# Optimization experiments

Measured on AMD Instinct MI355X. Metric: run time of the kernel, lower is better.

Reference implementation:

```python
import jax, jax.numpy as jnp
import numpy as np

B, D_IN, D_OUT = 8192, 1024, 1024


def setup_inputs() -> dict:
    key = jax.random.key(0)
    k1, k2 = jax.random.split(key)
    x = jax.random.normal(k1, (B, D_IN), dtype=jnp.float32)
    # Keras add_weight(shape=(3, input_dim, output_dim), initializer='uniform')
    kernel = jax.random.normal(k2, (3, D_IN, D_OUT), dtype=jnp.float32) * 0.05
    return {"x": x, "kernel": kernel}


def reference(x, kernel):
    # x: (B, D). Layer does expand_dims(axis=1) -> (B, 1, D) (seq_len == 1).
    output_dim = kernel.shape[-1]
    xe = x[:, None, :]                                   # (B, 1, D)
    q = jnp.einsum('bsd,do->bso', xe, kernel[0])         # (B, 1, O)
    k = jnp.einsum('bsd,do->bso', xe, kernel[1])         # (B, 1, O)
    v = jnp.einsum('bsd,do->bso', xe, kernel[2])         # (B, 1, O)
    scores = jnp.einsum('bqo,bko->bqk', q, k) / jnp.sqrt(
        jnp.asarray(output_dim, x.dtype))                # (B, 1, 1)
    attn = jax.nn.softmax(scores, axis=-1)
    out = jnp.einsum('bqk,bko->bqo', attn, v)            # (B, 1, O)
    return out
```

## Files before the change

### kernel.cpp

```cpp
#include <hip/hip_runtime.h>
#include <hip/hip_bf16.h>
#include <stdint.h>

#define AS1 __attribute__((address_space(1)))
#define AS3 __attribute__((address_space(3)))

typedef __attribute__((ext_vector_type(8))) short bf16x8_t;
typedef __attribute__((ext_vector_type(4))) float f32x4_t;

#define DDIM 1024
#define WT_ELEMS ((size_t)DDIM * DDIM)
#define XB_ELEMS ((size_t)8192 * DDIM)

static __device__ inline ushort f32_to_bf16_rne(float f) {
  union { float f; uint32_t u; } v;
  v.f = f;
  v.u += 0x7FFFu + ((v.u >> 16) & 1u);
  return (ushort)(v.u >> 16);
}

__global__ __launch_bounds__(256) void transpose_w(const float* __restrict__ W,
                                                   ushort* __restrict__ Wt) {
  __shared__ float tile[64][65];
  const int t  = threadIdx.x;
  const int bk = blockIdx.x;
  const int bn = blockIdx.y;
#pragma unroll
  for (int s = 0; s < 4; ++s) {
    const int slot = (s << 8) + t;
    const int r    = slot >> 4;
    const int c4   = (slot & 15) << 2;
    const float4 v = *(const float4*)(W + (size_t)(bk * 64 + r) * DDIM + bn * 64 + c4);
    tile[r][c4 + 0] = v.x; tile[r][c4 + 1] = v.y;
    tile[r][c4 + 2] = v.z; tile[r][c4 + 3] = v.w;
  }
  __syncthreads();
#pragma unroll
  for (int s = 0; s < 2; ++s) {
    const int slot = (s << 8) + t;
    const int n    = slot >> 3;
    const int k8   = (slot & 7) << 3;
    union { ushort h[8]; uint4 u; } tmp;
#pragma unroll
    for (int j = 0; j < 8; ++j) tmp.h[j] = f32_to_bf16_rne(tile[k8 + j][n]);
    *(uint4*)(Wt + (size_t)(bn * 64 + n) * DDIM + bk * 64 + k8) = tmp.u;
  }
}

__global__ __launch_bounds__(256) void convert_x(const float* __restrict__ X,
                                                 ushort* __restrict__ Xb) {
  const size_t i = ((size_t)blockIdx.x * 256 + threadIdx.x) << 3;
  const float4 v0 = *(const float4*)(X + i);
  const float4 v1 = *(const float4*)(X + i + 4);
  union { ushort h[8]; uint4 u; } o;
  o.h[0] = f32_to_bf16_rne(v0.x); o.h[1] = f32_to_bf16_rne(v0.y);
  o.h[2] = f32_to_bf16_rne(v0.z); o.h[3] = f32_to_bf16_rne(v0.w);
  o.h[4] = f32_to_bf16_rne(v1.x); o.h[5] = f32_to_bf16_rne(v1.y);
  o.h[6] = f32_to_bf16_rne(v1.z); o.h[7] = f32_to_bf16_rne(v1.w);
  *(uint4*)(Xb + i) = o.u;
}

__global__ __launch_bounds__(256, 4) void gemm_bb(const ushort* __restrict__ Xb,
                                                  const ushort* __restrict__ Wt,
                                                  float* __restrict__ C) {
  __shared__ __align__(16) ushort As[64 * 32];
  __shared__ __align__(16) ushort Bs[128 * 32];

  const int t    = threadIdx.x;
  const int wave = t >> 6;
  const int lane = t & 63;
  const int m0 = blockIdx.x * 64;
  const int n0 = blockIdx.y * 128;

  const int s  = (wave << 6) + lane;
  const int sr = s >> 2;
  const int sc = (s & 3) ^ ((sr >> 1) & 3);
  const ushort* aptr  = Xb + (size_t)(m0 + sr) * DDIM + (sc << 3);
  const ushort* bptr0 = Wt + (size_t)(n0 + sr) * DDIM + (sc << 3);
  const ushort* bptr1 = Wt + (size_t)(n0 + 64 + sr) * DDIM + (sc << 3);

  AS3 char* ldsA = (AS3 char*)As;
  AS3 char* ldsB = (AS3 char*)Bs;
  const int woff = wave << 10;

  const int wr = (wave >> 1) << 5;
  const int wc = (wave & 1) << 6;
  const int fr = lane & 15;
  const int fq = lane >> 4;

  f32x4_t acc[2][4] = {};

  for (int kt = 0; kt < DDIM; kt += 32) {
    __syncthreads();
    __builtin_amdgcn_global_load_lds((const AS1 void*)aptr,  (AS3 void*)(ldsA + woff),        16, 0, 0);
    __builtin_amdgcn_global_load_lds((const AS1 void*)bptr0, (AS3 void*)(ldsB + woff),        16, 0, 0);
    __builtin_amdgcn_global_load_lds((const AS1 void*)bptr1, (AS3 void*)(ldsB + 4096 + woff), 16, 0, 0);
    aptr += 32; bptr0 += 32; bptr1 += 32;
    __syncthreads();

    bf16x8_t af[2], bfr[4];
#pragma unroll
    for (int mi = 0; mi < 2; ++mi) {
      const int r = wr + (mi << 4) + fr;
      af[mi] = *(const bf16x8_t*)&As[(r << 5) + ((fq ^ ((r >> 1) & 3)) << 3)];
    }
#pragma unroll
    for (int ni = 0; ni < 4; ++ni) {
      const int r = wc + (ni << 4) + fr;
      bfr[ni] = *(const bf16x8_t*)&Bs[(r << 5) + ((fq ^ ((r >> 1) & 3)) << 3)];
    }
#pragma unroll
    for (int mi = 0; mi < 2; ++mi)
#pragma unroll
      for (int ni = 0; ni < 4; ++ni)
        acc[mi][ni] = __builtin_amdgcn_mfma_f32_16x16x32_bf16(af[mi], bfr[ni], acc[mi][ni], 0, 0, 0);
  }

#pragma unroll
  for (int mi = 0; mi < 2; ++mi) {
#pragma unroll
    for (int r = 0; r < 4; ++r) {
      const int row = m0 + wr + (mi << 4) + (fq << 2) + r;
      float* crow = C + (size_t)row * DDIM + n0 + wc + fr;
#pragma unroll
      for (int ni = 0; ni < 4; ++ni)
        crow[ni << 4] = acc[mi][ni][r];
    }
  }
}

__global__ __launch_bounds__(256) void gemm_xw(const float* __restrict__ X,
                                               const ushort* __restrict__ Wt,
                                               float* __restrict__ C) {
  __shared__ __align__(16) ushort As[128 * 32];
  __shared__ __align__(16) ushort Bs[128 * 32];
  const int t    = threadIdx.x;
  const int wave = t >> 6;
  const int lane = t & 63;
  const int m0 = blockIdx.x * 128;
  const int n0 = blockIdx.y * 128;
  const int srow  = (wave << 4) + (lane >> 2);
  const int skcol = (lane & 3) << 3;
  const ushort* bptr0 = Wt + (size_t)(n0 + srow) * DDIM + skcol;
  const ushort* bptr1 = Wt + (size_t)(n0 + 64 + srow) * DDIM + skcol;
  const int ar = t >> 2;
  const int ak = (t & 3) << 3;
  const float* aptr0 = X + (size_t)(m0 + ar) * DDIM + ak;
  const float* aptr1 = X + (size_t)(m0 + 64 + ar) * DDIM + ak;
  ushort* asw0 = &As[(ar << 5) + ak];
  ushort* asw1 = &As[((ar + 64) << 5) + ak];
  const int wr = (wave >> 1) << 6;
  const int wc = (wave & 1) << 6;
  const int fr = lane & 15;
  const int fq = lane >> 4;
  f32x4_t acc[4][4] = {};
  AS3 char* ldsB = (AS3 char*)Bs;
  const int woff = wave << 10;
  for (int kt = 0; kt < DDIM; kt += 32) {
    const float4 a00 = *(const float4*)(aptr0);
    const float4 a01 = *(const float4*)(aptr0 + 4);
    const float4 a10 = *(const float4*)(aptr1);
    const float4 a11 = *(const float4*)(aptr1 + 4);
    aptr0 += 32; aptr1 += 32;
    __syncthreads();
    __builtin_amdgcn_global_load_lds((const AS1 void*)bptr0, (AS3 void*)(ldsB + woff),        16, 0, 0);
    __builtin_amdgcn_global_load_lds((const AS1 void*)bptr1, (AS3 void*)(ldsB + 4096 + woff), 16, 0, 0);
    bptr0 += 32; bptr1 += 32;
    union { ushort h[8]; bf16x8_t v; } c0, c1;
    c0.h[0] = f32_to_bf16_rne(a00.x); c0.h[1] = f32_to_bf16_rne(a00.y);
    c0.h[2] = f32_to_bf16_rne(a00.z); c0.h[3] = f32_to_bf16_rne(a00.w);
    c0.h[4] = f32_to_bf16_rne(a01.x); c0.h[5] = f32_to_bf16_rne(a01.y);
    c0.h[6] = f32_to_bf16_rne(a01.z); c0.h[7] = f32_to_bf16_rne(a01.w);
    c1.h[0] = f32_to_bf16_rne(a10.x); c1.h[1] = f32_to_bf16_rne(a10.y);
    c1.h[2] = f32_to_bf16_rne(a10.z); c1.h[3] = f32_to_bf16_rne(a10.w);
    c1.h[4] = f32_to_bf16_rne(a11.x); c1.h[5] = f32_to_bf16_rne(a11.y);
    c1.h[6] = f32_to_bf16_rne(a11.z); c1.h[7] = f32_to_bf16_rne(a11.w);
    *(bf16x8_t*)asw0 = c0.v;
    *(bf16x8_t*)asw1 = c1.v;
    __syncthreads();
    bf16x8_t af[4], bfr[4];
#pragma unroll
    for (int mi = 0; mi < 4; ++mi)
      af[mi] = *(const bf16x8_t*)&As[((wr + (mi << 4) + fr) << 5) + (fq << 3)];
#pragma unroll
    for (int ni = 0; ni < 4; ++ni)
      bfr[ni] = *(const bf16x8_t*)&Bs[((wc + (ni << 4) + fr) << 5) + (fq << 3)];
#pragma unroll
    for (int mi = 0; mi < 4; ++mi)
#pragma unroll
      for (int ni = 0; ni < 4; ++ni)
        acc[mi][ni] = __builtin_amdgcn_mfma_f32_16x16x32_bf16(af[mi], bfr[ni], acc[mi][ni], 0, 0, 0);
  }
#pragma unroll
  for (int mi = 0; mi < 4; ++mi)
#pragma unroll
    for (int r = 0; r < 4; ++r) {
      const int row = m0 + wr + (mi << 4) + (fq << 2) + r;
      float* crow = C + (size_t)row * DDIM + n0 + wc + fr;
#pragma unroll
      for (int ni = 0; ni < 4; ++ni)
        crow[ni << 4] = acc[mi][ni][r];
    }
}

extern "C" void kernel_launch(void* const* d_in, const int* in_sizes, int n_in,
                              void* d_out, int out_size, void* d_ws, size_t ws_size,
                              hipStream_t stream) {
  const float* x    = (const float*)d_in[0];
  const float* kern = (const float*)d_in[1];
  const float* W = kern + (size_t)2 * DDIM * DDIM;
  ushort* Wt = (ushort*)d_ws;
  const int M = in_sizes[0] / DDIM;

  transpose_w<<<dim3(DDIM / 64, DDIM / 64), 256, 0, stream>>>(W, Wt);

  if (ws_size >= (WT_ELEMS + XB_ELEMS) * sizeof(ushort)) {
    ushort* Xb = (ushort*)d_ws + WT_ELEMS;
    convert_x<<<(unsigned)((size_t)M * DDIM / 8 / 256), 256, 0, stream>>>(x, Xb);
    gemm_bb<<<dim3(M / 64, DDIM / 128), 256, 0, stream>>>(Xb, Wt, (float*)d_out);
  } else {
    gemm_xw<<<dim3(M / 128, DDIM / 128), 256, 0, stream>>>(x, Wt, (float*)d_out);
  }
}
```

Measured before the change: 117.8 us.

## Enlarge bf16 GEMM tile to 128x128 with double-buffered K=64 LDS stages

Moves the bf16 GEMM from 64x128 tiles with K=32 steps to 128x128 tiles with K=64 steps. Global-to-LDS loads for the next stage are issued while the current stage is computed, leaving one barrier per iteration instead of two. The LDS swizzle becomes 8-way to match the wider rows. The aim is more data reuse per loaded byte and less barrier overhead, at the cost of 64KB of LDS per block and lower occupancy.

```diff
diff --git a/kernel.cpp b/kernel.cpp
--- a/kernel.cpp
+++ b/kernel.cpp
@@ -60,64 +60,82 @@
   *(uint4*)(Xb + i) = o.u;
 }
 
-__global__ __launch_bounds__(256, 4) void gemm_bb(const ushort* __restrict__ Xb,
+__global__ __launch_bounds__(256, 2) void gemm_bb(const ushort* __restrict__ Xb,
                                                   const ushort* __restrict__ Wt,
                                                   float* __restrict__ C) {
-  __shared__ __align__(16) ushort As[64 * 32];
-  __shared__ __align__(16) ushort Bs[128 * 32];
+  __shared__ __align__(16) ushort As[2][128 * 64];
+  __shared__ __align__(16) ushort Bs[2][128 * 64];
 
   const int t    = threadIdx.x;
   const int wave = t >> 6;
   const int lane = t & 63;
-  const int m0 = blockIdx.x * 64;
+  const int m0 = blockIdx.x * 128;
   const int n0 = blockIdx.y * 128;
 
-  const int s  = (wave << 6) + lane;
-  const int sr = s >> 2;
-  const int sc = (s & 3) ^ ((sr >> 1) & 3);
-  const ushort* aptr  = Xb + (size_t)(m0 + sr) * DDIM + (sc << 3);
-  const ushort* bptr0 = Wt + (size_t)(n0 + sr) * DDIM + (sc << 3);
-  const ushort* bptr1 = Wt + (size_t)(n0 + 64 + sr) * DDIM + (sc << 3);
-
-  AS3 char* ldsA = (AS3 char*)As;
-  AS3 char* ldsB = (AS3 char*)Bs;
+  const int sr = t >> 3;
+  const int sc = (t & 7) ^ (sr & 7);
+  const ushort* aB = Xb + (size_t)(m0 + sr) * DDIM + (sc << 3);
+  const ushort* bB = Wt + (size_t)(n0 + sr) * DDIM + (sc << 3);
+
+  AS3 char* lA = (AS3 char*)&As[0][0];
+  AS3 char* lB = (AS3 char*)&Bs[0][0];
   const int woff = wave << 10;
 
-  const int wr = (wave >> 1) << 5;
+  const int wr = (wave >> 1) << 6;
   const int wc = (wave & 1) << 6;
   const int fr = lane & 15;
   const int fq = lane >> 4;
 
-  f32x4_t acc[2][4] = {};
-
-  for (int kt = 0; kt < DDIM; kt += 32) {
+  f32x4_t acc[4][4] = {};
+
+  auto issue = [&](int kt, int p) {
+    const ushort* a = aB + kt;
+    const ushort* b = bB + kt;
+    AS3 char* dA = lA + (p << 14) + woff;
+    AS3 char* dB = lB + (p << 14) + woff;
+#pragma unroll
+    for (int j = 0; j < 4; ++j) {
+      __builtin_amdgcn_global_load_lds((const AS1 void*)(a + (size_t)(j << 5) * DDIM),
+                                       (AS3 void*)(dA + (j << 12)), 16, 0, 0);
+      __builtin_amdgcn_global_load_lds((const AS1 void*)(b + (size_t)(j << 5) * DDIM),
+                                       (AS3 void*)(dB + (j << 12)), 16, 0, 0);
+    }
+  };
+
+  issue(0, 0);
+  __syncthreads();
+
+  for (int i = 0; i < 16; ++i) {
+    const int p = i & 1;
+    if (i < 15) issue((i + 1) << 6, p ^ 1);
+
+    const ushort* Ab = &As[p][0];
+    const ushort* Bb = &Bs[p][0];
+#pragma unroll
+    for (int ks = 0; ks < 2; ++ks) {
+      const int kc = (ks << 2) + fq;
+      bf16x8_t af[4], bfr[4];
+#pragma unroll
+      for (int mi = 0; mi < 4; ++mi) {
+        const int r = wr + (mi << 4) + fr;
+        af[mi] = *(const bf16x8_t*)&Ab[(r << 6) + ((kc ^ (r & 7)) << 3)];
+      }
+#pragma unroll
+      for (int ni = 0; ni < 4; ++ni) {
+        const int r = wc + (ni << 4) + fr;
+        bfr[ni] = *(const bf16x8_t*)&Bb[(r << 6) + ((kc ^ (r & 7)) << 3)];
+      }
+#pragma unroll
+      for (int mi = 0; mi < 4; ++mi)
+#pragma unroll
+        for (int ni = 0; ni < 4; ++ni)
+          acc[mi][ni] = __builtin_amdgcn_mfma_f32_16x16x32_bf16(af[mi], bfr[ni], acc[mi][ni], 0, 0, 0);
+    }
     __syncthreads();
-    __builtin_amdgcn_global_load_lds((const AS1 void*)aptr,  (AS3 void*)(ldsA + woff),        16, 0, 0);
-    __builtin_amdgcn_global_load_lds((const AS1 void*)bptr0, (AS3 void*)(ldsB + woff),        16, 0, 0);
-    __builtin_amdgcn_global_load_lds((const AS1 void*)bptr1, (AS3 void*)(ldsB + 4096 + woff), 16, 0, 0);
-    aptr += 32; bptr0 += 32; bptr1 += 32;
-    __syncthreads();
-
-    bf16x8_t af[2], bfr[4];
-#pragma unroll
-    for (int mi = 0; mi < 2; ++mi) {
-      const int r = wr + (mi << 4) + fr;
-      af[mi] = *(const bf16x8_t*)&As[(r << 5) + ((fq ^ ((r >> 1) & 3)) << 3)];
-    }
-#pragma unroll
-    for (int ni = 0; ni < 4; ++ni) {
-      const int r = wc + (ni << 4) + fr;
-      bfr[ni] = *(const bf16x8_t*)&Bs[(r << 5) + ((fq ^ ((r >> 1) & 3)) << 3)];
-    }
-#pragma unroll
-    for (int mi = 0; mi < 2; ++mi)
-#pragma unroll
-      for (int ni = 0; ni < 4; ++ni)
-        acc[mi][ni] = __builtin_amdgcn_mfma_f32_16x16x32_bf16(af[mi], bfr[ni], acc[mi][ni], 0, 0, 0);
-  }
-
-#pragma unroll
-  for (int mi = 0; mi < 2; ++mi) {
+  }
+
+#pragma unroll
+  for (int mi = 0; mi < 4; ++mi) {
 #pragma unroll
     for (int r = 0; r < 4; ++r) {
       const int row = m0 + wr + (mi << 4) + (fq << 2) + r;
@@ -217,7 +235,7 @@
   if (ws_size >= (WT_ELEMS + XB_ELEMS) * sizeof(ushort)) {
     ushort* Xb = (ushort*)d_ws + WT_ELEMS;
     convert_x<<<(unsigned)((size_t)M * DDIM / 8 / 256), 256, 0, stream>>>(x, Xb);
-    gemm_bb<<<dim3(M / 64, DDIM / 128), 256, 0, stream>>>(Xb, Wt, (float*)d_out);
+    gemm_bb<<<dim3(M / 128, DDIM / 128), 256, 0, stream>>>(Xb, Wt, (float*)d_out);
   } else {
     gemm_xw<<<dim3(M / 128, DDIM / 128), 256, 0, stream>>>(x, Wt, (float*)d_out);
   }
```

Result: faster. 111.5 us (-5.4%).

## Pre-swizzle X and W into MFMA fragment layout and load directly to registers

Applied to the files above, without the earlier changes.

Merges the X conversion and the W transpose into one prep kernel. That kernel writes both operands in the per-lane MFMA fragment order. The GEMM then skips LDS and syncthreads: each wave loads its fragments straight from global memory into registers, double-buffered across k-steps, with a 128x128 tile and 4x4 accumulators per wave. The aim is to remove LDS traffic, barriers and one launch. The trade-off is that each wave re-reads fragments from global/L2 with no block-level sharing, and register pressure goes up.

```diff
diff --git a/kernel.cpp b/kernel.cpp
--- a/kernel.cpp
+++ b/kernel.cpp
@@ -17,6 +17,136 @@
   v.f = f;
   v.u += 0x7FFFu + ((v.u >> 16) & 1u);
   return (ushort)(v.u >> 16);
+}
+
+
+__global__ __launch_bounds__(256) void prep(const float* __restrict__ X,
+                                            const float* __restrict__ W,
+                                            ushort* __restrict__ FA,
+                                            ushort* __restrict__ FB,
+                                            int nx) {
+  __shared__ ushort xbuf[16][1032];
+  __shared__ float  wtile[64][65];
+  const int t = threadIdx.x;
+
+  if ((int)blockIdx.x < nx) {
+    const int m16 = blockIdx.x;
+    const float* src = X + (size_t)m16 * 16 * DDIM;
+#pragma unroll
+    for (int rep = 0; rep < 16; ++rep) {
+      const int fl = ((rep << 8) + t) << 2;
+      const float4 v = *(const float4*)(src + fl);
+      const int r = fl >> 10, c = fl & 1023;
+      xbuf[r][c + 0] = f32_to_bf16_rne(v.x);
+      xbuf[r][c + 1] = f32_to_bf16_rne(v.y);
+      xbuf[r][c + 2] = f32_to_bf16_rne(v.z);
+      xbuf[r][c + 3] = f32_to_bf16_rne(v.w);
+    }
+    __syncthreads();
+    ushort* dst = FA + (size_t)m16 * 16384;
+#pragma unroll
+    for (int rep = 0; rep < 8; ++rep) {
+      const int e    = (rep << 8) + t;
+      const int k32  = e >> 6;
+      const int lane = e & 63;
+      const int fr   = lane & 15, fq = lane >> 4;
+      const uint4 u = *(const uint4*)&xbuf[fr][(k32 << 5) + (fq << 3)];
+      *(uint4*)(dst + (size_t)e * 8) = u;
+    }
+    return;
+  }
+
+  const int bid = (int)blockIdx.x - nx;
+  const int bk = bid & 15;
+  const int bn = bid >> 4;
+#pragma unroll
+  for (int s = 0; s < 4; ++s) {
+    const int slot = (s << 8) + t;
+    const int r    = slot >> 4;
+    const int c4   = (slot & 15) << 2;
+    const float4 v = *(const float4*)(W + (size_t)(bk * 64 + r) * DDIM + bn * 64 + c4);
+    wtile[r][c4 + 0] = v.x; wtile[r][c4 + 1] = v.y;
+    wtile[r][c4 + 2] = v.z; wtile[r][c4 + 3] = v.w;
+  }
+  __syncthreads();
+#pragma unroll
+  for (int rep = 0; rep < 2; ++rep) {
+    const int e    = (rep << 8) + t;
+    const int lane = e & 63;
+    const int gh   = e >> 6;
+    const int g = gh >> 1, h = gh & 1;
+    const int fr = lane & 15, fq = lane >> 4;
+    const int lkb = (h << 5) + (fq << 3);
+    union { ushort h8[8]; uint4 u; } tmp;
+#pragma unroll
+    for (int j = 0; j < 8; ++j)
+      tmp.h8[j] = f32_to_bf16_rne(wtile[lkb + j][(g << 4) + fr]);
+    const size_t n16 = (size_t)(bn << 2) + g;
+    const size_t k32 = (size_t)(bk << 1) + h;
+    *(uint4*)(FB + (n16 * 32 + k32) * 512 + (size_t)lane * 8) = tmp.u;
+  }
+}
+
+__global__ __launch_bounds__(256, 2) void gemm_frag(const ushort* __restrict__ FA,
+                                                    const ushort* __restrict__ FB,
+                                                    float* __restrict__ C) {
+  const int t    = threadIdx.x;
+  const int wave = t >> 6;
+  const int lane = t & 63;
+  const int m0 = blockIdx.x * 128;
+  const int n0 = blockIdx.y * 128;
+  const int wr = (wave >> 1) << 6;
+  const int wc = (wave & 1) << 6;
+  const int fr = lane & 15;
+  const int fq = lane >> 4;
+
+  const ushort* pa = FA + (size_t)((m0 + wr) >> 4) * 16384 + (size_t)lane * 8;
+  const ushort* pb = FB + (size_t)((n0 + wc) >> 4) * 16384 + (size_t)lane * 8;
+
+  bf16x8_t a0[4], b0[4], a1[4], b1[4];
+  f32x4_t acc[4][4] = {};
+
+#define LD(ar, br, s)                                                          \
+  {                                                                            \
+    const ushort* qa = pa + (size_t)(s) * 512;                                 \
+    const ushort* qb = pb + (size_t)(s) * 512;                                 \
+    _Pragma("unroll") for (int i = 0; i < 4; ++i)                              \
+        (ar)[i] = *(const bf16x8_t*)(qa + (size_t)i * 16384);                  \
+    _Pragma("unroll") for (int i = 0; i < 4; ++i)                              \
+        (br)[i] = *(const bf16x8_t*)(qb + (size_t)i * 16384);                  \
+  }
+#define MM(ar, br)                                                             \
+  {                                                                            \
+    _Pragma("unroll") for (int mi = 0; mi < 4; ++mi)                           \
+        _Pragma("unroll") for (int ni = 0; ni < 4; ++ni)                       \
+            acc[mi][ni] = __builtin_amdgcn_mfma_f32_16x16x32_bf16(             \
+                (ar)[mi], (br)[ni], acc[mi][ni], 0, 0, 0);                     \
+  }
+
+  LD(a0, b0, 0);
+  for (int s2 = 0; s2 < 15; ++s2) {
+    LD(a1, b1, 2 * s2 + 1);
+    MM(a0, b0);
+    LD(a0, b0, 2 * s2 + 2);
+    MM(a1, b1);
+  }
+  LD(a1, b1, 31);
+  MM(a0, b0);
+  MM(a1, b1);
+#undef LD
+#undef MM
+
+#pragma unroll
+  for (int mi = 0; mi < 4; ++mi) {
+#pragma unroll
+    for (int r = 0; r < 4; ++r) {
+      const int row = m0 + wr + (mi << 4) + (fq << 2) + r;
+      float* crow = C + (size_t)row * DDIM + n0 + wc + fr;
+#pragma unroll
+      for (int ni = 0; ni < 4; ++ni)
+        crow[ni << 4] = acc[mi][ni][r];
+    }
+  }
 }
 
 __global__ __launch_bounds__(256) void transpose_w(const float* __restrict__ W,
@@ -44,88 +174,6 @@
 #pragma unroll
     for (int j = 0; j < 8; ++j) tmp.h[j] = f32_to_bf16_rne(tile[k8 + j][n]);
     *(uint4*)(Wt + (size_t)(bn * 64 + n) * DDIM + bk * 64 + k8) = tmp.u;
-  }
-}
-
-__global__ __launch_bounds__(256) void convert_x(const float* __restrict__ X,
-                                                 ushort* __restrict__ Xb) {
-  const size_t i = ((size_t)blockIdx.x * 256 + threadIdx.x) << 3;
-  const float4 v0 = *(const float4*)(X + i);
-  const float4 v1 = *(const float4*)(X + i + 4);
-  union { ushort h[8]; uint4 u; } o;
-  o.h[0] = f32_to_bf16_rne(v0.x); o.h[1] = f32_to_bf16_rne(v0.y);
-  o.h[2] = f32_to_bf16_rne(v0.z); o.h[3] = f32_to_bf16_rne(v0.w);
-  o.h[4] = f32_to_bf16_rne(v1.x); o.h[5] = f32_to_bf16_rne(v1.y);
-  o.h[6] = f32_to_bf16_rne(v1.z); o.h[7] = f32_to_bf16_rne(v1.w);
-  *(uint4*)(Xb + i) = o.u;
-}
-
-__global__ __launch_bounds__(256, 4) void gemm_bb(const ushort* __restrict__ Xb,
-                                                  const ushort* __restrict__ Wt,
-                                                  float* __restrict__ C) {
-  __shared__ __align__(16) ushort As[64 * 32];
-  __shared__ __align__(16) ushort Bs[128 * 32];
-
-  const int t    = threadIdx.x;
-  const int wave = t >> 6;
-  const int lane = t & 63;
-  const int m0 = blockIdx.x * 64;
-  const int n0 = blockIdx.y * 128;
-
-  const int s  = (wave << 6) + lane;
-  const int sr = s >> 2;
-  const int sc = (s & 3) ^ ((sr >> 1) & 3);
-  const ushort* aptr  = Xb + (size_t)(m0 + sr) * DDIM + (sc << 3);
-  const ushort* bptr0 = Wt + (size_t)(n0 + sr) * DDIM + (sc << 3);
-  const ushort* bptr1 = Wt + (size_t)(n0 + 64 + sr) * DDIM + (sc << 3);
-
-  AS3 char* ldsA = (AS3 char*)As;
-  AS3 char* ldsB = (AS3 char*)Bs;
-  const int woff = wave << 10;
-
-  const int wr = (wave >> 1) << 5;
-  const int wc = (wave & 1) << 6;
-  const int fr = lane & 15;
-  const int fq = lane >> 4;
-
-  f32x4_t acc[2][4] = {};
-
-  for (int kt = 0; kt < DDIM; kt += 32) {
-    __syncthreads();
-    __builtin_amdgcn_global_load_lds((const AS1 void*)aptr,  (AS3 void*)(ldsA + woff),        16, 0, 0);
-    __builtin_amdgcn_global_load_lds((const AS1 void*)bptr0, (AS3 void*)(ldsB + woff),        16, 0, 0);
-    __builtin_amdgcn_global_load_lds((const AS1 void*)bptr1, (AS3 void*)(ldsB + 4096 + woff), 16, 0, 0);
-    aptr += 32; bptr0 += 32; bptr1 += 32;
-    __syncthreads();
-
-    bf16x8_t af[2], bfr[4];
-#pragma unroll
-    for (int mi = 0; mi < 2; ++mi) {
-      const int r = wr + (mi << 4) + fr;
-      af[mi] = *(const bf16x8_t*)&As[(r << 5) + ((fq ^ ((r >> 1) & 3)) << 3)];
-    }
-#pragma unroll
-    for (int ni = 0; ni < 4; ++ni) {
-      const int r = wc + (ni << 4) + fr;
-      bfr[ni] = *(const bf16x8_t*)&Bs[(r << 5) + ((fq ^ ((r >> 1) & 3)) << 3)];
-    }
-#pragma unroll
-    for (int mi = 0; mi < 2; ++mi)
-#pragma unroll
-      for (int ni = 0; ni < 4; ++ni)
-        acc[mi][ni] = __builtin_amdgcn_mfma_f32_16x16x32_bf16(af[mi], bfr[ni], acc[mi][ni], 0, 0, 0);
-  }
-
-#pragma unroll
-  for (int mi = 0; mi < 2; ++mi) {
-#pragma unroll
-    for (int r = 0; r < 4; ++r) {
-      const int row = m0 + wr + (mi << 4) + (fq << 2) + r;
-      float* crow = C + (size_t)row * DDIM + n0 + wc + fr;
-#pragma unroll
-      for (int ni = 0; ni < 4; ++ni)
-        crow[ni << 4] = acc[mi][ni][r];
-    }
   }
 }
 
@@ -209,16 +257,17 @@
   const float* x    = (const float*)d_in[0];
   const float* kern = (const float*)d_in[1];
   const float* W = kern + (size_t)2 * DDIM * DDIM;
-  ushort* Wt = (ushort*)d_ws;
   const int M = in_sizes[0] / DDIM;
 
-  transpose_w<<<dim3(DDIM / 64, DDIM / 64), 256, 0, stream>>>(W, Wt);
-
   if (ws_size >= (WT_ELEMS + XB_ELEMS) * sizeof(ushort)) {
-    ushort* Xb = (ushort*)d_ws + WT_ELEMS;
-    convert_x<<<(unsigned)((size_t)M * DDIM / 8 / 256), 256, 0, stream>>>(x, Xb);
-    gemm_bb<<<dim3(M / 64, DDIM / 128), 256, 0, stream>>>(Xb, Wt, (float*)d_out);
+    ushort* FA = (ushort*)d_ws;
+    ushort* FB = (ushort*)d_ws + XB_ELEMS;
+    const int nx = M / 16;
+    prep<<<nx + 256, 256, 0, stream>>>(x, W, FA, FB, nx);
+    gemm_frag<<<dim3(M / 128, DDIM / 128), 256, 0, stream>>>(FA, FB, (float*)d_out);
   } else {
+    ushort* Wt = (ushort*)d_ws;
+    transpose_w<<<dim3(16, 16), 256, 0, stream>>>(W, Wt);
     gemm_xw<<<dim3(M / 128, DDIM / 128), 256, 0, stream>>>(x, Wt, (float*)d_out);
   }
 }
```

Measured after the change: 115.2 us. -2.2%, faster.
